# Kernel tuning notes

Measured on AMD Instinct MI355X. Metric: run time of the kernel, lower is better.

## Reference

```python
import jax, jax.numpy as jnp
import numpy as np

ALPHA = 0.1
BETA = 0.3
MARGIN = 2.0


def setup_inputs() -> dict:
    key = jax.random.key(0)
    k1, k2 = jax.random.split(key)
    prediction = jax.random.normal(k1, (8, 2048, 512), dtype=jnp.float32)
    target_seg = jax.random.randint(k2, (8, 2048), 0, 16, dtype=jnp.int64)
    return {"prediction": prediction, "target_seg": target_seg}


def _pairwise_sqdist(x):
    # x: [n, L, d] -> squared Euclidean distances [n, L, L] via a GEMM
    sq = jnp.sum(x * x, axis=-1)  # [n, L]
    inner = jnp.einsum('nld,nmd->nlm', x, x)  # [n, L, L]
    d2 = sq[:, :, None] + sq[:, None, :] - 2.0 * inner
    return jnp.maximum(d2, 0.0)


def _safe_sqrt(d2):
    # sqrt with zero (not NaN) gradient at 0, matching torch.cdist behavior
    pos = d2 > 0
    return jnp.where(pos, jnp.sqrt(jnp.where(pos, d2, 1.0)), 0.0)


def reference(prediction, target_seg):
    # y[i,j,k] = 1 if target_seg[i,j] == target_seg[i,k]
    y = (target_seg[:, :, None] == target_seg[:, None, :]).astype(prediction.dtype)
    d2 = _pairwise_sqdist(prediction)
    dist = _safe_sqrt(d2)
    hinge = jnp.maximum(MARGIN - dist, 0.0)
    loss = ALPHA * y * d2 + BETA * (1.0 - y) * hinge * hinge
    return jnp.mean(loss)
```

## Files before the change

kernel.cpp:

```cpp
#include <hip/hip_runtime.h>
#include <hip/hip_fp8.h>
#include <math.h>

#define L      2048
#define DDIM   512
#define NBATCH 8
#define BM     128
#define BN     128
#define NTILE  (L / BM)
#define NPAIR  (NTILE * (NTILE + 1) / 2)
#define TOTAL_BLOCKS (NBATCH * NPAIR)

#define PANSZ  16384

#define ALPHA  0.1f
#define BETA   0.3f
#define MARGIN 2.0f

typedef __attribute__((ext_vector_type(16))) float f32x16;
typedef long long2v __attribute__((ext_vector_type(2)));

__global__ __launch_bounds__(256) void conv_kernel(const float* __restrict__ pred,
                                                   unsigned char* __restrict__ h,
                                                   float* __restrict__ sq) {
    int w     = threadIdx.x >> 6;
    int lane  = threadIdx.x & 63;
    int batch = blockIdx.x & 7;
    int idx   = blockIdx.x >> 3;
    int row   = batch * L + idx * 4 + w;
    const float* p = pred + (size_t)row * DDIM + lane * 8;
    float4 v0 = *(const float4*)(p);
    float4 v1 = *(const float4*)(p + 4);
    float vals[8] = {v0.x, v0.y, v0.z, v0.w, v1.x, v1.y, v1.z, v1.w};
    unsigned q[8];
    float s = 0.0f;
    #pragma unroll
    for (int i = 0; i < 8; ++i) {
        float x = vals[i];
        s = fmaf(x, x, s);
        __hip_fp8_e4m3 f8(x);
        q[i] = (unsigned)f8.__x;
    }
    unsigned lo = q[0] | (q[1] << 8) | (q[2] << 16) | (q[3] << 24);
    unsigned hi = q[4] | (q[5] << 8) | (q[6] << 16) | (q[7] << 24);
    int r5    = row & 31;
    int pair  = lane >> 2;
    int khalf = lane & 1;
    int kodd  = (lane >> 1) & 1;
    size_t off = (size_t)(row >> 5) * PANSZ + pair * 1024
               + (r5 + 32 * khalf) * 16 + kodd * 8;
    *(uint2*)(h + off) = make_uint2(lo, hi);
    #pragma unroll
    for (int o = 32; o > 0; o >>= 1) s += __shfl_down(s, o);
    if (lane == 0) sq[row] = s;
}

__global__ __launch_bounds__(256) void loss_kernel(
        const unsigned char* __restrict__ h,
        const int*   __restrict__ seg,
        const float* __restrict__ sq,
        double*      __restrict__ partials) {
    __shared__ double wred[4];

    int bid = blockIdx.x;
    int n = bid & 7;
    int p = bid >> 3;
    int tj = 0;
    while (true) {
        int rl2 = NTILE - tj;
        if (p < rl2) break;
        p -= rl2;
        ++tj;
    }
    int tk = tj + p;

    int t    = threadIdx.x;
    int wid  = t >> 6;
    int lane = t & 63;
    int wr   = wid >> 1, wc = wid & 1;
    int l31  = lane & 31;
    int hsel = lane >> 5;

    const unsigned char* base = h + (size_t)n * L * DDIM;

    const unsigned char* pa0 = base + (size_t)(tj * 4 + wr * 2 + 0) * PANSZ + lane * 16;
    const unsigned char* pa1 = base + (size_t)(tj * 4 + wr * 2 + 1) * PANSZ + lane * 16;
    const unsigned char* pb0 = base + (size_t)(tk * 4 + wc * 2 + 0) * PANSZ + lane * 16;
    const unsigned char* pb1 = base + (size_t)(tk * 4 + wc * 2 + 1) * PANSZ + lane * 16;

    f32x16 acc[2][2];
    #pragma unroll
    for (int m = 0; m < 2; ++m)
        #pragma unroll
        for (int nf = 0; nf < 2; ++nf)
            #pragma unroll
            for (int x = 0; x < 16; ++x) acc[m][nf][x] = 0.0f;

    long2v ra0[3], ra1[3], rb0[3], rb1[3];
    #pragma unroll
    for (int q = 0; q < 3; ++q) {
        ra0[q] = *(const long2v*)(pa0 + q * 1024);
        ra1[q] = *(const long2v*)(pa1 + q * 1024);
        rb0[q] = *(const long2v*)(pb0 + q * 1024);
        rb1[q] = *(const long2v*)(pb1 + q * 1024);
    }

    #pragma unroll
    for (int ks2 = 0; ks2 < 16; ++ks2) {
        const int slot = ks2 % 3;
        long2v a0 = ra0[slot], a1 = ra1[slot];
        long2v b0 = rb0[slot], b1 = rb1[slot];

        acc[0][0] = __builtin_amdgcn_mfma_f32_32x32x16_fp8_fp8(a0.x, b0.x, acc[0][0], 0, 0, 0);
        acc[0][1] = __builtin_amdgcn_mfma_f32_32x32x16_fp8_fp8(a0.x, b1.x, acc[0][1], 0, 0, 0);
        acc[1][0] = __builtin_amdgcn_mfma_f32_32x32x16_fp8_fp8(a1.x, b0.x, acc[1][0], 0, 0, 0);
        acc[1][1] = __builtin_amdgcn_mfma_f32_32x32x16_fp8_fp8(a1.x, b1.x, acc[1][1], 0, 0, 0);
        acc[0][0] = __builtin_amdgcn_mfma_f32_32x32x16_fp8_fp8(a0.y, b0.y, acc[0][0], 0, 0, 0);
        acc[0][1] = __builtin_amdgcn_mfma_f32_32x32x16_fp8_fp8(a0.y, b1.y, acc[0][1], 0, 0, 0);
        acc[1][0] = __builtin_amdgcn_mfma_f32_32x32x16_fp8_fp8(a1.y, b0.y, acc[1][0], 0, 0, 0);
        acc[1][1] = __builtin_amdgcn_mfma_f32_32x32x16_fp8_fp8(a1.y, b1.y, acc[1][1], 0, 0, 0);

        if (ks2 + 3 < 16) {
            ra0[slot] = *(const long2v*)(pa0 + (ks2 + 3) * 1024);
            ra1[slot] = *(const long2v*)(pa1 + (ks2 + 3) * 1024);
            rb0[slot] = *(const long2v*)(pb0 + (ks2 + 3) * 1024);
            rb1[slot] = *(const long2v*)(pb1 + (ks2 + 3) * 1024);
        }
    }

    const int*   segb = seg + n * L;
    const float* sqb  = sq + n * L;
    int j0 = tj * BM, k0 = tk * BN;

    float lsum = 0.0f;
    #pragma unroll
    for (int nf = 0; nf < 2; ++nf) {
        int k = k0 + wc * 64 + nf * 32 + l31;
        float sqk = sqb[k];
        int   sgk = segb[k];
        #pragma unroll
        for (int m = 0; m < 2; ++m)
            #pragma unroll
            for (int x = 0; x < 16; ++x) {
                int j = j0 + wr * 64 + m * 32 + (x & 3) + 8 * (x >> 2) + 4 * hsel;
                if (j > k) continue;
                float inner = acc[m][nf][x];
                float d2 = fmaxf(sqb[j] + sqk - 2.0f * inner, 0.0f);
                float v;
                if (segb[j] == sgk) {
                    v = ALPHA * d2;
                } else {
                    float dist = sqrtf(d2);
                    float hg = fmaxf(MARGIN - dist, 0.0f);
                    v = BETA * hg * hg;
                }
                lsum += (j < k) ? 2.0f * v : v;
            }
    }

    double wgt = 1.0;
    double dsum = (double)lsum * wgt;
    #pragma unroll
    for (int off = 32; off > 0; off >>= 1)
        dsum += __shfl_down(dsum, off);
    if (lane == 0) wred[wid] = dsum;
    __syncthreads();
    if (t == 0) partials[bid] = (wred[0] + wred[1]) + (wred[2] + wred[3]);
}

__global__ __launch_bounds__(256) void reduce_kernel(const double* __restrict__ partials,
                                                     float* __restrict__ out,
                                                     int nPart, double invCount) {
    __shared__ double red[256];
    int t = threadIdx.x;
    double s = 0.0;
    for (int i = t; i < nPart; i += 256) s += partials[i];
    red[t] = s;
    __syncthreads();
    #pragma unroll
    for (int k = 128; k > 0; k >>= 1) {
        if (t < k) red[t] += red[t + k];
        __syncthreads();
    }
    if (t == 0) out[0] = (float)(red[0] * invCount);
}

extern "C" void kernel_launch(void* const* d_in, const int* in_sizes, int n_in,
                              void* d_out, int out_size, void* d_ws, size_t ws_size,
                              hipStream_t stream) {
    const float* pred = (const float*)d_in[0];
    const int*   seg  = (const int*)d_in[1];
    float* out = (float*)d_out;

    const size_t HALF = (size_t)NBATCH * L * DDIM;
    unsigned char* h  = (unsigned char*)d_ws;
    float*  sq        = (float*)(h + HALF);
    double* partials  = (double*)(sq + NBATCH * L);

    conv_kernel<<<NBATCH * L / 4, 256, 0, stream>>>(pred, h, sq);
    loss_kernel<<<TOTAL_BLOCKS, 256, 0, stream>>>(h, seg, sq, partials);
    reduce_kernel<<<1, 256, 0, stream>>>(partials, out, TOTAL_BLOCKS,
                                         1.0 / (double)((size_t)NBATCH * L * L));
}
```

Measured before the change: 55.50 us.

## Compute same-segment loss analytically and screen hinge pairs with a 64-dim fp8 GEMM

The same-segment term is now computed in closed form from per-segment sums and sums of squares (2*count*T - 2*||S||^2), so it no longer needs a pairwise GEMM. The hinge term is nonzero only when the distance is below the margin. It is screened with an fp8 GEMM over just the first 64 dimensions, because a prefix distance lower-bounds the full distance. A slack term scaled by the norms covers fp8 rounding error. Surviving pairs are recomputed exactly in fp32 and summed with fixed-point 64-bit atomics. This cuts GEMM work roughly eightfold. The risks are that the screening slack may be too small and drop real pairs, and a slow scalar fallback path if many pairs pass the screen.

```diff
diff --git a/kernel.cpp b/kernel.cpp
--- a/kernel.cpp
+++ b/kernel.cpp
@@ -5,30 +5,75 @@
 #define L      2048
 #define DDIM   512
 #define NBATCH 8
-#define BM     128
-#define BN     128
-#define NTILE  (L / BM)
+#define NTILE  16
 #define NPAIR  (NTILE * (NTILE + 1) / 2)
-#define TOTAL_BLOCKS (NBATCH * NPAIR)
-
-#define PANSZ  16384
-
-#define ALPHA  0.1f
-#define BETA   0.3f
-#define MARGIN 2.0f
+#define SCREEN_BLOCKS (NBATCH * NPAIR)
+
+#define ALPHA  0.1
+#define BETA   0.3
+#define PAN2   2048
 
 typedef __attribute__((ext_vector_type(16))) float f32x16;
 typedef long long2v __attribute__((ext_vector_type(2)));
 
-__global__ __launch_bounds__(256) void conv_kernel(const float* __restrict__ pred,
-                                                   unsigned char* __restrict__ h,
-                                                   float* __restrict__ sq) {
-    int w     = threadIdx.x >> 6;
-    int lane  = threadIdx.x & 63;
-    int batch = blockIdx.x & 7;
-    int idx   = blockIdx.x >> 3;
-    int row   = batch * L + idx * 4 + w;
-    const float* p = pred + (size_t)row * DDIM + lane * 8;
+__global__ __launch_bounds__(256) void gsum_kernel(const float* __restrict__ pred,
+                                                   const int*   __restrict__ seg,
+                                                   float* __restrict__ Spart,
+                                                   float* __restrict__ Tpart) {
+    __shared__ float Sl[8][16][32];
+    __shared__ float Tl[8][16][32];
+    int bid  = blockIdx.x;
+    int n    = bid & 7;
+    int c    = (bid >> 3) & 15;
+    int half = bid >> 7;
+    int t = threadIdx.x;
+    int d = t & 31, p = t >> 5;
+
+    for (int i = t; i < 8 * 16 * 32; i += 256) {
+        ((float*)Sl)[i] = 0.0f;
+        ((float*)Tl)[i] = 0.0f;
+    }
+    __syncthreads();
+
+    const float* pb   = pred + (size_t)n * L * DDIM + c * 32 + d;
+    const int*   segb = seg + n * L + half * 1024;
+    #pragma unroll 4
+    for (int i = 0; i < 128; ++i) {
+        int lr  = i * 8 + p;
+        int row = half * 1024 + lr;
+        float x = pb[(size_t)row * DDIM];
+        int g   = segb[lr];
+        Sl[p][g][d] += x;
+        Tl[p][g][d] += x * x;
+    }
+    __syncthreads();
+
+    for (int i = t; i < 512; i += 256) {
+        int g = i >> 5, dd = i & 31;
+        float s = 0.0f, tt = 0.0f;
+        #pragma unroll
+        for (int q = 0; q < 8; ++q) { s += Sl[q][g][dd]; tt += Tl[q][g][dd]; }
+        Spart[((size_t)bid * 16 + g) * 32 + dd] = s;
+        Sl[0][g][dd] = tt;
+    }
+    __syncthreads();
+    if (t < 16) {
+        float tt = 0.0f;
+        #pragma unroll
+        for (int dd = 0; dd < 32; ++dd) tt += Sl[0][t][dd];
+        Tpart[bid * 16 + t] = tt;
+    }
+}
+
+__global__ __launch_bounds__(256) void conv64_kernel(const float* __restrict__ pred,
+                                                     unsigned char* __restrict__ h8,
+                                                     float* __restrict__ sq64,
+                                                     float* __restrict__ n64) {
+    int t    = threadIdx.x;
+    int rowl = t >> 3;
+    int d8   = t & 7;
+    int row  = blockIdx.x * 32 + rowl;
+    const float* p = pred + (size_t)row * DDIM + d8 * 8;
     float4 v0 = *(const float4*)(p);
     float4 v1 = *(const float4*)(p + 4);
     float vals[8] = {v0.x, v0.y, v0.z, v0.w, v1.x, v1.y, v1.z, v1.w};
@@ -43,25 +88,25 @@
     }
     unsigned lo = q[0] | (q[1] << 8) | (q[2] << 16) | (q[3] << 24);
     unsigned hi = q[4] | (q[5] << 8) | (q[6] << 16) | (q[7] << 24);
-    int r5    = row & 31;
-    int pair  = lane >> 2;
-    int khalf = lane & 1;
-    int kodd  = (lane >> 1) & 1;
-    size_t off = (size_t)(row >> 5) * PANSZ + pair * 1024
-               + (r5 + 32 * khalf) * 16 + kodd * 8;
-    *(uint2*)(h + off) = make_uint2(lo, hi);
-    #pragma unroll
-    for (int o = 32; o > 0; o >>= 1) s += __shfl_down(s, o);
-    if (lane == 0) sq[row] = s;
-}
-
-__global__ __launch_bounds__(256) void loss_kernel(
-        const unsigned char* __restrict__ h,
+    int pair  = d8 >> 2;
+    int kodd  = (d8 >> 1) & 1;
+    int khalf = d8 & 1;
+    size_t off = (size_t)blockIdx.x * PAN2 + pair * 1024
+               + ((row & 31) + 32 * khalf) * 16 + kodd * 8;
+    *(uint2*)(h8 + off) = make_uint2(lo, hi);
+    s += __shfl_down(s, 4);
+    s += __shfl_down(s, 2);
+    s += __shfl_down(s, 1);
+    if (d8 == 0) { sq64[row] = s; n64[row] = sqrtf(s); }
+}
+
+__global__ __launch_bounds__(256) void screen_kernel(
+        const unsigned char* __restrict__ h8,
+        const float* __restrict__ sq64,
+        const float* __restrict__ n64,
         const int*   __restrict__ seg,
-        const float* __restrict__ sq,
-        double*      __restrict__ partials) {
-    __shared__ double wred[4];
-
+        const float* __restrict__ pred,
+        unsigned long long* __restrict__ hacc) {
     int bid = blockIdx.x;
     int n = bid & 7;
     int p = bid >> 3;
@@ -81,12 +126,10 @@
     int l31  = lane & 31;
     int hsel = lane >> 5;
 
-    const unsigned char* base = h + (size_t)n * L * DDIM;
-
-    const unsigned char* pa0 = base + (size_t)(tj * 4 + wr * 2 + 0) * PANSZ + lane * 16;
-    const unsigned char* pa1 = base + (size_t)(tj * 4 + wr * 2 + 1) * PANSZ + lane * 16;
-    const unsigned char* pb0 = base + (size_t)(tk * 4 + wc * 2 + 0) * PANSZ + lane * 16;
-    const unsigned char* pb1 = base + (size_t)(tk * 4 + wc * 2 + 1) * PANSZ + lane * 16;
+    const unsigned char* pa0 = h8 + (size_t)(n * 64 + tj * 4 + wr * 2 + 0) * PAN2 + lane * 16;
+    const unsigned char* pa1 = pa0 + PAN2;
+    const unsigned char* pb0 = h8 + (size_t)(n * 64 + tk * 4 + wc * 2 + 0) * PAN2 + lane * 16;
+    const unsigned char* pb1 = pb0 + PAN2;
 
     f32x16 acc[2][2];
     #pragma unroll
@@ -96,21 +139,12 @@
             #pragma unroll
             for (int x = 0; x < 16; ++x) acc[m][nf][x] = 0.0f;
 
-    long2v ra0[3], ra1[3], rb0[3], rb1[3];
-    #pragma unroll
-    for (int q = 0; q < 3; ++q) {
-        ra0[q] = *(const long2v*)(pa0 + q * 1024);
-        ra1[q] = *(const long2v*)(pa1 + q * 1024);
-        rb0[q] = *(const long2v*)(pb0 + q * 1024);
-        rb1[q] = *(const long2v*)(pb1 + q * 1024);
-    }
-
-    #pragma unroll
-    for (int ks2 = 0; ks2 < 16; ++ks2) {
-        const int slot = ks2 % 3;
-        long2v a0 = ra0[slot], a1 = ra1[slot];
-        long2v b0 = rb0[slot], b1 = rb1[slot];
-
+    #pragma unroll
+    for (int ks2 = 0; ks2 < 2; ++ks2) {
+        long2v a0 = *(const long2v*)(pa0 + ks2 * 1024);
+        long2v a1 = *(const long2v*)(pa1 + ks2 * 1024);
+        long2v b0 = *(const long2v*)(pb0 + ks2 * 1024);
+        long2v b1 = *(const long2v*)(pb1 + ks2 * 1024);
         acc[0][0] = __builtin_amdgcn_mfma_f32_32x32x16_fp8_fp8(a0.x, b0.x, acc[0][0], 0, 0, 0);
         acc[0][1] = __builtin_amdgcn_mfma_f32_32x32x16_fp8_fp8(a0.x, b1.x, acc[0][1], 0, 0, 0);
         acc[1][0] = __builtin_amdgcn_mfma_f32_32x32x16_fp8_fp8(a1.x, b0.x, acc[1][0], 0, 0, 0);
@@ -119,70 +153,95 @@
         acc[0][1] = __builtin_amdgcn_mfma_f32_32x32x16_fp8_fp8(a0.y, b1.y, acc[0][1], 0, 0, 0);
         acc[1][0] = __builtin_amdgcn_mfma_f32_32x32x16_fp8_fp8(a1.y, b0.y, acc[1][0], 0, 0, 0);
         acc[1][1] = __builtin_amdgcn_mfma_f32_32x32x16_fp8_fp8(a1.y, b1.y, acc[1][1], 0, 0, 0);
-
-        if (ks2 + 3 < 16) {
-            ra0[slot] = *(const long2v*)(pa0 + (ks2 + 3) * 1024);
-            ra1[slot] = *(const long2v*)(pa1 + (ks2 + 3) * 1024);
-            rb0[slot] = *(const long2v*)(pb0 + (ks2 + 3) * 1024);
-            rb1[slot] = *(const long2v*)(pb1 + (ks2 + 3) * 1024);
-        }
-    }
-
-    const int*   segb = seg + n * L;
-    const float* sqb  = sq + n * L;
-    int j0 = tj * BM, k0 = tk * BN;
-
-    float lsum = 0.0f;
+    }
+
+    const int*   segb  = seg + n * L;
+    const float* sqb   = sq64 + n * L;
+    const float* nb    = n64 + n * L;
+
     #pragma unroll
     for (int nf = 0; nf < 2; ++nf) {
-        int k = k0 + wc * 64 + nf * 32 + l31;
+        int k = tk * 128 + wc * 64 + nf * 32 + l31;
         float sqk = sqb[k];
+        float nk  = nb[k];
         int   sgk = segb[k];
         #pragma unroll
         for (int m = 0; m < 2; ++m)
             #pragma unroll
             for (int x = 0; x < 16; ++x) {
-                int j = j0 + wr * 64 + m * 32 + (x & 3) + 8 * (x >> 2) + 4 * hsel;
-                if (j > k) continue;
-                float inner = acc[m][nf][x];
-                float d2 = fmaxf(sqb[j] + sqk - 2.0f * inner, 0.0f);
-                float v;
-                if (segb[j] == sgk) {
-                    v = ALPHA * d2;
-                } else {
-                    float dist = sqrtf(d2);
-                    float hg = fmaxf(MARGIN - dist, 0.0f);
-                    v = BETA * hg * hg;
+                int j = tj * 128 + wr * 64 + m * 32 + (x & 3) + 8 * (x >> 2) + 4 * hsel;
+                if (j >= k) continue;
+                if (segb[j] == sgk) continue;
+                float d2e = sqb[j] + sqk - 2.0f * acc[m][nf][x];
+                float thr = 4.5f + 0.27f * nb[j] * nk;
+                if (d2e >= thr) continue;
+                const float* pj = pred + (size_t)(n * L + j) * DDIM;
+                const float* pk2 = pred + (size_t)(n * L + k) * DDIM;
+                float d2x = 0.0f;
+                for (int d = 0; d < DDIM; ++d) {
+                    float df = pj[d] - pk2[d];
+                    d2x = fmaf(df, df, d2x);
                 }
-                lsum += (j < k) ? 2.0f * v : v;
+                if (d2x < 4.0f) {
+                    float dist = sqrtf(d2x);
+                    float hg = 2.0f - dist;
+                    double v = (double)hg * (double)hg * 2.0 * 1073741824.0;
+                    atomicAdd(hacc, (unsigned long long)(long long)(v + 0.5));
+                }
             }
     }
-
-    double wgt = 1.0;
-    double dsum = (double)lsum * wgt;
-    #pragma unroll
-    for (int off = 32; off > 0; off >>= 1)
-        dsum += __shfl_down(dsum, off);
-    if (lane == 0) wred[wid] = dsum;
-    __syncthreads();
-    if (t == 0) partials[bid] = (wred[0] + wred[1]) + (wred[2] + wred[3]);
-}
-
-__global__ __launch_bounds__(256) void reduce_kernel(const double* __restrict__ partials,
-                                                     float* __restrict__ out,
-                                                     int nPart, double invCount) {
+}
+
+__global__ __launch_bounds__(256) void final_kernel(const float* __restrict__ Spart,
+                                                    const float* __restrict__ Tpart,
+                                                    const int*   __restrict__ seg,
+                                                    const unsigned long long* __restrict__ hacc,
+                                                    float* __restrict__ out) {
+    __shared__ int cl[8][16];
     __shared__ double red[256];
     int t = threadIdx.x;
-    double s = 0.0;
-    for (int i = t; i < nPart; i += 256) s += partials[i];
-    red[t] = s;
-    __syncthreads();
-    #pragma unroll
-    for (int k = 128; k > 0; k >>= 1) {
-        if (t < k) red[t] += red[t + k];
+    if (t < 128) ((int*)cl)[t] = 0;
+    __syncthreads();
+    for (int i = t; i < NBATCH * L; i += 256) {
+        int n = i >> 11;
+        atomicAdd(&cl[n][seg[i]], 1);
+    }
+    __syncthreads();
+
+    double acc = 0.0;
+    for (int i = t; i < 8 * 16 * 512; i += 256) {
+        int dg = i & 511, g = (i >> 9) & 15, n = i >> 13;
+        int c = dg >> 5, dd = dg & 31;
+        int bid0 = c * 8 + n;
+        int bid1 = bid0 + 128;
+        float s = Spart[((size_t)bid0 * 16 + g) * 32 + dd]
+                + Spart[((size_t)bid1 * 16 + g) * 32 + dd];
+        acc -= 2.0 * (double)s * (double)s;
+    }
+    if (t < 128) {
+        int n = t >> 4, g = t & 15;
+        double T = 0.0;
+        #pragma unroll
+        for (int c = 0; c < 16; ++c) {
+            T += (double)Tpart[(c * 8 + n) * 16 + g];
+            T += (double)Tpart[(c * 8 + n + 128) * 16 + g];
+        }
+        acc += 2.0 * (double)cl[n][g] * T;
+    }
+    red[t] = acc;
+    __syncthreads();
+    #pragma unroll
+    for (int s2 = 128; s2 > 0; s2 >>= 1) {
+        if (t < s2) red[t] += red[t + s2];
         __syncthreads();
     }
-    if (t == 0) out[0] = (float)(red[0] * invCount);
+    if (t == 0) {
+        double same  = red[0];
+        double hinge = (double)(long long)hacc[0] / 1073741824.0;
+        double loss  = (ALPHA * same + BETA * hinge)
+                     / ((double)NBATCH * (double)L * (double)L);
+        out[0] = (float)loss;
+    }
 }
 
 extern "C" void kernel_launch(void* const* d_in, const int* in_sizes, int n_in,
@@ -192,13 +251,16 @@
     const int*   seg  = (const int*)d_in[1];
     float* out = (float*)d_out;
 
-    const size_t HALF = (size_t)NBATCH * L * DDIM;
-    unsigned char* h  = (unsigned char*)d_ws;
-    float*  sq        = (float*)(h + HALF);
-    double* partials  = (double*)(sq + NBATCH * L);
-
-    conv_kernel<<<NBATCH * L / 4, 256, 0, stream>>>(pred, h, sq);
-    loss_kernel<<<TOTAL_BLOCKS, 256, 0, stream>>>(h, seg, sq, partials);
-    reduce_kernel<<<1, 256, 0, stream>>>(partials, out, TOTAL_BLOCKS,
-                                         1.0 / (double)((size_t)NBATCH * L * L));
-}
+    unsigned char* h8   = (unsigned char*)d_ws;
+    float* sq64         = (float*)(h8 + 512 * PAN2);
+    float* n64          = sq64 + NBATCH * L;
+    float* Spart        = n64 + NBATCH * L;
+    float* Tpart        = Spart + 256 * 16 * 32;
+    unsigned long long* hacc = (unsigned long long*)(Tpart + 256 * 16);
+
+    hipMemsetAsync(hacc, 0, sizeof(unsigned long long), stream);
+    gsum_kernel<<<256, 256, 0, stream>>>(pred, seg, Spart, Tpart);
+    conv64_kernel<<<512, 256, 0, stream>>>(pred, h8, sq64, n64);
+    screen_kernel<<<SCREEN_BLOCKS, 256, 0, stream>>>(h8, sq64, n64, seg, pred, hacc);
+    final_kernel<<<1, 256, 0, stream>>>(Spart, Tpart, seg, hacc, out);
+}
```

Measured after the change: 144.5 us. 2.6x slower.
